# Kernel tuning notes

Measured on AMD Instinct MI355X. Metric: run time of the kernel, lower is better.

The kernel has to match this reference:

```python
import jax, jax.numpy as jnp
import numpy as np

B, DIM, H, W = 64, 256, 5, 5


def setup_inputs() -> dict:
    key = jax.random.key(0)
    k1 = jax.random.fold_in(key, 1)
    feat_map = jax.random.normal(k1, (B, DIM, H, W), dtype=jnp.float32)
    # nn.Parameter init: log(1 / (2 * h * w)) * ones(1, 1)
    temperature = jnp.full((1, 1), float(np.log(1.0 / (2 * H * W))), dtype=jnp.float32)
    return {"feat_map": feat_map, "temperature": temperature}


def reference(feat_map, temperature):
    # comp_relation with lego=False, normalize_bdc=True, out_map=False, no_diag=False
    b, d, h, w = feat_map.shape
    f = feat_map.reshape(b, d, h * w)                     # [B, d, hw]
    # pairwise channel correlation: sum_p |f_i + f_j| - |f_i - f_j|
    s_plus = jnp.sum(jnp.abs(f[:, :, None, :] + f[:, None, :, :]), axis=-1)   # [B, d, d]
    s_minus = jnp.sum(jnp.abs(f[:, :, None, :] - f[:, None, :, :]), axis=-1)  # [B, d, d]
    out = (s_plus - s_minus) * 0.5 * jnp.exp(temperature[0, 0])
    # centering: out - (1/d) out @ ones - (1/d) ones @ out
    row_mean = jnp.sum(out, axis=2, keepdims=True) / d    # (out @ I_M) / d, broadcast over cols
    col_mean = jnp.sum(out, axis=1, keepdims=True) / d    # (I_M @ out) / d, broadcast over rows
    out = out - row_mean - col_mean
    # Triuvec (including diagonal), row-major order as in torch nonzero of triu mask
    iu, ju = jnp.triu_indices(d)
    return out[:, iu, ju]                                 # [B, d*(d+1)/2]
```

## Files before the change

kernel.cpp:

```cpp
#include <hip/hip_runtime.h>
#include <math.h>

#define NB   64
#define D    256
#define HW   25
#define TRI  32896
#define TS   64
#define PSTR 68

__device__ __forceinline__ void tile_bands(int t, int& bi, int& bj) {
    bi = (t < 4) ? 0 : (t < 7) ? 1 : (t < 9) ? 2 : 3;
    const int o4 = (bi == 0) ? 0 : (bi == 1) ? 4 : (bi == 2) ? 7 : 9;
    bj = bi + (t - o4);
}

__global__ __launch_bounds__(256) void tile_kernel(const float* __restrict__ feat,
                                                   float* __restrict__ rsp,
                                                   float* __restrict__ out) {
    __shared__ __align__(16) float as[HW * PSTR];
    __shared__ __align__(16) float bs[HW * PSTR];
    __shared__ float red[2][TS][17];

    const int tid = threadIdx.x;
    const int blk = blockIdx.x;
    const int b   = blk / 10;
    const int t   = blk - b * 10;
    int bi, bj; tile_bands(t, bi, bj);
    const int ibase = bi * TS, jbase = bj * TS;
    const bool diag = (bi == bj);

    const float* fb = feat + (size_t)b * D * HW;

    for (int idx = tid; idx < TS * HW; idx += 256) {
        int r = idx / HW;
        int p = idx - r * HW;
        as[p * PSTR + r] = fb[(ibase + r) * HW + p];
        bs[p * PSTR + r] = fb[(jbase + r) * HW + p];
    }
    __syncthreads();

    const int tx = tid & 15;
    const int ty = tid >> 4;

    float acc[4][4] = {{0.f}};
#pragma unroll 5
    for (int p = 0; p < HW; ++p) {
        float4 av = *reinterpret_cast<const float4*>(&as[p * PSTR + ty * 4]);
        float4 bv = *reinterpret_cast<const float4*>(&bs[p * PSTR + tx * 4]);
        float a4[4] = {av.x, av.y, av.z, av.w};
        float b4[4] = {bv.x, bv.y, bv.z, bv.w};
#pragma unroll
        for (int r = 0; r < 4; ++r)
#pragma unroll
            for (int q = 0; q < 4; ++q)
                acc[r][q] += fabsf(a4[r] + b4[q]) - fabsf(a4[r] - b4[q]);
    }

    float* ob = out + (size_t)b * TRI;
    if (diag) {
#pragma unroll
        for (int r = 0; r < 4; ++r) {
            const int i = ibase + ty * 4 + r;
            const int rowoff = (i * (513 - i)) >> 1;
#pragma unroll
            for (int q = 0; q < 4; ++q) {
                const int j = jbase + tx * 4 + q;
                if (j >= i) ob[rowoff + (j - i)] = acc[r][q];
            }
        }
    } else {
#pragma unroll
        for (int r = 0; r < 4; ++r) {
            const int i = ibase + ty * 4 + r;
            const int rowoff = (i * (513 - i)) >> 1;
#pragma unroll
            for (int q = 0; q < 4; ++q) {
                const int j = jbase + tx * 4 + q;
                ob[rowoff + (j - i)] = acc[r][q];
            }
        }
    }

    float pi[4];
#pragma unroll
    for (int r = 0; r < 4; ++r) pi[r] = acc[r][0] + acc[r][1] + acc[r][2] + acc[r][3];
#pragma unroll
    for (int r = 0; r < 4; ++r) red[0][ty * 4 + r][tx] = pi[r];
    if (!diag) {
        float pj[4];
#pragma unroll
        for (int q = 0; q < 4; ++q) pj[q] = acc[0][q] + acc[1][q] + acc[2][q] + acc[3][q];
#pragma unroll
        for (int q = 0; q < 4; ++q) red[1][tx * 4 + q][ty] = pj[q];
    }
    __syncthreads();

    if (tid < TS) {
        float si = 0.f;
#pragma unroll
        for (int x = 0; x < 16; ++x) si += red[0][tid][x];
        rsp[((b * 4 + bi) * 4 + (bj - bi)) * TS + tid] = si;
        if (!diag) {
            float sj = 0.f;
#pragma unroll
            for (int x = 0; x < 16; ++x) sj += red[1][tid][x];
            rsp[((b * 4 + bj) * 4 + (4 - bj + bi)) * TS + tid] = sj;
        }
    }
}

__global__ __launch_bounds__(256) void center_kernel(const float* __restrict__ temp,
                                                     const float* __restrict__ rsp,
                                                     float* __restrict__ out) {
    __shared__ float rsum[2][TS];

    const int tid = threadIdx.x;
    const int blk = blockIdx.x;
    const int b   = blk / 10;
    const int t   = blk - b * 10;
    int bi, bj; tile_bands(t, bi, bj);
    const int ibase = bi * TS, jbase = bj * TS;
    const bool diag = (bi == bj);

    if (tid < TS) {
        float s = 0.f;
#pragma unroll
        for (int sl = 0; sl < 4; ++sl) s += rsp[((b * 4 + bi) * 4 + sl) * TS + tid];
        rsum[0][tid] = s;
    } else if (tid < 2 * TS) {
        const int il = tid - TS;
        float s = 0.f;
#pragma unroll
        for (int sl = 0; sl < 4; ++sl) s += rsp[((b * 4 + bj) * 4 + sl) * TS + il];
        rsum[1][il] = s;
    }
    __syncthreads();

    const int tx = tid & 15;
    const int ty = tid >> 4;
    const float sc = 0.5f * expf(temp[0]);
    float* ob = out + (size_t)b * TRI;

#pragma unroll
    for (int r = 0; r < 4; ++r) {
        const int i = ibase + ty * 4 + r;
        const int rowoff = (i * (513 - i)) >> 1;
        const float ri = rsum[0][ty * 4 + r];
#pragma unroll
        for (int q = 0; q < 4; ++q) {
            const int j = jbase + tx * 4 + q;
            if (!diag || j >= i) {
                float* p = &ob[rowoff + (j - i)];
                const float e = *p;
                *p = sc * (e - (ri + rsum[1][tx * 4 + q]) * (1.0f / 256.0f));
            }
        }
    }
}

extern "C" void kernel_launch(void* const* d_in, const int* in_sizes, int n_in,
                              void* d_out, int out_size, void* d_ws, size_t ws_size,
                              hipStream_t stream) {
    const float* feat = (const float*)d_in[0];
    const float* temp = (const float*)d_in[1];
    float* out = (float*)d_out;
    float* rsp = (float*)d_ws;

    tile_kernel<<<NB * 10, 256, 0, stream>>>(feat, rsp, out);
    center_kernel<<<NB * 10, 256, 0, stream>>>(temp, rsp, out);
}
```

Measured before the change: 28.54 us.

## Shrink tiles to 32x32 with 64-thread blocks for more parallel blocks

Moves from 64x64 tiles in 256-thread blocks (640 blocks) to 32x32 tiles in 64-thread blocks (2304 blocks), and rewrites the row-sum partial layout and triangular tile mapping to match. Diagonal tiles now reuse the A tile instead of loading B. The aim is to spread the small workload across more CUs and waves and to cut wasted work on diagonal tiles. The cost is more blocks, more redundant global loads of feature rows, and more partial sums to combine in the centering kernel.

Result: slower. 36.49 us (+27.8%).

```diff
diff --git a/kernel.cpp b/kernel.cpp
--- a/kernel.cpp
+++ b/kernel.cpp
@@ -5,48 +5,60 @@
 #define D    256
 #define HW   25
 #define TRI  32896
-#define TS   64
-#define PSTR 68
+#define BTS  32
+#define NT   36
+#define PST  36
 
-__device__ __forceinline__ void tile_bands(int t, int& bi, int& bj) {
-    bi = (t < 4) ? 0 : (t < 7) ? 1 : (t < 9) ? 2 : 3;
-    const int o4 = (bi == 0) ? 0 : (bi == 1) ? 4 : (bi == 2) ? 7 : 9;
-    bj = bi + (t - o4);
+__device__ __forceinline__ void tile_bands8(int t, int& bi, int& bj) {
+    int acc = 0;
+#pragma unroll
+    for (int w = 0; w < 8; ++w) {
+        const int cnt = 8 - w;
+        if (t < acc + cnt) { bi = w; bj = w + (t - acc); return; }
+        acc += cnt;
+    }
+    bi = 7; bj = 7;
 }
 
-__global__ __launch_bounds__(256) void tile_kernel(const float* __restrict__ feat,
-                                                   float* __restrict__ rsp,
-                                                   float* __restrict__ out) {
-    __shared__ __align__(16) float as[HW * PSTR];
-    __shared__ __align__(16) float bs[HW * PSTR];
-    __shared__ float red[2][TS][17];
+__global__ __launch_bounds__(64) void tile_kernel(const float* __restrict__ feat,
+                                                  float* __restrict__ rsp,
+                                                  float* __restrict__ out) {
+    __shared__ __align__(16) float as[HW * PST];
+    __shared__ __align__(16) float bs[HW * PST];
+    __shared__ float red0[BTS][9];
+    __shared__ float red1[BTS][9];
 
     const int tid = threadIdx.x;
     const int blk = blockIdx.x;
-    const int b   = blk / 10;
-    const int t   = blk - b * 10;
-    int bi, bj; tile_bands(t, bi, bj);
-    const int ibase = bi * TS, jbase = bj * TS;
+    const int b   = blk / NT;
+    const int t   = blk - b * NT;
+    int bi, bj; tile_bands8(t, bi, bj);
+    const int ibase = bi * BTS, jbase = bj * BTS;
     const bool diag = (bi == bj);
 
     const float* fb = feat + (size_t)b * D * HW;
 
-    for (int idx = tid; idx < TS * HW; idx += 256) {
-        int r = idx / HW;
-        int p = idx - r * HW;
-        as[p * PSTR + r] = fb[(ibase + r) * HW + p];
-        bs[p * PSTR + r] = fb[(jbase + r) * HW + p];
+    for (int idx = tid; idx < BTS * HW; idx += 64) {
+        const int r = idx / HW, p = idx - r * HW;
+        as[p * PST + r] = fb[(ibase + r) * HW + p];
+    }
+    if (!diag) {
+        for (int idx = tid; idx < BTS * HW; idx += 64) {
+            const int r = idx / HW, p = idx - r * HW;
+            bs[p * PST + r] = fb[(jbase + r) * HW + p];
+        }
     }
     __syncthreads();
 
-    const int tx = tid & 15;
-    const int ty = tid >> 4;
+    const float* bsp = diag ? as : bs;
+    const int tx = tid & 7;
+    const int ty = tid >> 3;
 
     float acc[4][4] = {{0.f}};
-#pragma unroll 5
+#pragma unroll
     for (int p = 0; p < HW; ++p) {
-        float4 av = *reinterpret_cast<const float4*>(&as[p * PSTR + ty * 4]);
-        float4 bv = *reinterpret_cast<const float4*>(&bs[p * PSTR + tx * 4]);
+        float4 av = *reinterpret_cast<const float4*>(&as[p * PST + ty * 4]);
+        float4 bv = *reinterpret_cast<const float4*>(&bsp[p * PST + tx * 4]);
         float a4[4] = {av.x, av.y, av.z, av.w};
         float b4[4] = {bv.x, bv.y, bv.z, bv.w};
 #pragma unroll
@@ -85,59 +97,60 @@
 #pragma unroll
     for (int r = 0; r < 4; ++r) pi[r] = acc[r][0] + acc[r][1] + acc[r][2] + acc[r][3];
 #pragma unroll
-    for (int r = 0; r < 4; ++r) red[0][ty * 4 + r][tx] = pi[r];
+    for (int r = 0; r < 4; ++r) red0[ty * 4 + r][tx] = pi[r];
     if (!diag) {
         float pj[4];
 #pragma unroll
         for (int q = 0; q < 4; ++q) pj[q] = acc[0][q] + acc[1][q] + acc[2][q] + acc[3][q];
 #pragma unroll
-        for (int q = 0; q < 4; ++q) red[1][tx * 4 + q][ty] = pj[q];
+        for (int q = 0; q < 4; ++q) red1[tx * 4 + q][ty] = pj[q];
     }
     __syncthreads();
 
-    if (tid < TS) {
-        float si = 0.f;
+    if (tid < BTS) {
+        float s = 0.f;
 #pragma unroll
-        for (int x = 0; x < 16; ++x) si += red[0][tid][x];
-        rsp[((b * 4 + bi) * 4 + (bj - bi)) * TS + tid] = si;
-        if (!diag) {
-            float sj = 0.f;
+        for (int x = 0; x < 8; ++x) s += red0[tid][x];
+        rsp[((b * 8 + bi) * 8 + (bj - bi)) * BTS + tid] = s;
+    } else if (!diag) {
+        const int c = tid - BTS;
+        float s = 0.f;
 #pragma unroll
-            for (int x = 0; x < 16; ++x) sj += red[1][tid][x];
-            rsp[((b * 4 + bj) * 4 + (4 - bj + bi)) * TS + tid] = sj;
-        }
+        for (int x = 0; x < 8; ++x) s += red1[c][x];
+        rsp[((b * 8 + bj) * 8 + (8 - bj + bi)) * BTS + c] = s;
     }
 }
 
-__global__ __launch_bounds__(256) void center_kernel(const float* __restrict__ temp,
-                                                     const float* __restrict__ rsp,
-                                                     float* __restrict__ out) {
-    __shared__ float rsum[2][TS];
+__global__ __launch_bounds__(64) void center_kernel(const float* __restrict__ temp,
+                                                    const float* __restrict__ rsp,
+                                                    float* __restrict__ out) {
+    __shared__ float rsum0[BTS];
+    __shared__ float rsum1[BTS];
 
     const int tid = threadIdx.x;
     const int blk = blockIdx.x;
-    const int b   = blk / 10;
-    const int t   = blk - b * 10;
-    int bi, bj; tile_bands(t, bi, bj);
-    const int ibase = bi * TS, jbase = bj * TS;
+    const int b   = blk / NT;
+    const int t   = blk - b * NT;
+    int bi, bj; tile_bands8(t, bi, bj);
+    const int ibase = bi * BTS, jbase = bj * BTS;
     const bool diag = (bi == bj);
 
-    if (tid < TS) {
+    if (tid < BTS) {
         float s = 0.f;
 #pragma unroll
-        for (int sl = 0; sl < 4; ++sl) s += rsp[((b * 4 + bi) * 4 + sl) * TS + tid];
-        rsum[0][tid] = s;
-    } else if (tid < 2 * TS) {
-        const int il = tid - TS;
+        for (int sl = 0; sl < 8; ++sl) s += rsp[((b * 8 + bi) * 8 + sl) * BTS + tid];
+        rsum0[tid] = s;
+    } else {
+        const int c = tid - BTS;
         float s = 0.f;
 #pragma unroll
-        for (int sl = 0; sl < 4; ++sl) s += rsp[((b * 4 + bj) * 4 + sl) * TS + il];
-        rsum[1][il] = s;
+        for (int sl = 0; sl < 8; ++sl) s += rsp[((b * 8 + bj) * 8 + sl) * BTS + c];
+        rsum1[c] = s;
     }
     __syncthreads();
 
-    const int tx = tid & 15;
-    const int ty = tid >> 4;
+    const int tx = tid & 7;
+    const int ty = tid >> 3;
     const float sc = 0.5f * expf(temp[0]);
     float* ob = out + (size_t)b * TRI;
 
@@ -145,14 +158,14 @@
     for (int r = 0; r < 4; ++r) {
         const int i = ibase + ty * 4 + r;
         const int rowoff = (i * (513 - i)) >> 1;
-        const float ri = rsum[0][ty * 4 + r];
+        const float ri = rsum0[ty * 4 + r];
 #pragma unroll
         for (int q = 0; q < 4; ++q) {
             const int j = jbase + tx * 4 + q;
             if (!diag || j >= i) {
                 float* p = &ob[rowoff + (j - i)];
                 const float e = *p;
-                *p = sc * (e - (ri + rsum[1][tx * 4 + q]) * (1.0f / 256.0f));
+                *p = sc * (e - (ri + rsum1[tx * 4 + q]) * (1.0f / 256.0f));
             }
         }
     }
@@ -166,6 +179,6 @@
     float* out = (float*)d_out;
     float* rsp = (float*)d_ws;
 
-    tile_kernel<<<NB * 10, 256, 0, stream>>>(feat, rsp, out);
-    center_kernel<<<NB * 10, 256, 0, stream>>>(temp, rsp, out);
+    tile_kernel<<<NB * NT, 64, 0, stream>>>(feat, rsp, out);
+    center_kernel<<<NB * NT, 64, 0, stream>>>(temp, rsp, out);
 }
```

## Fuse tile and centering kernels with per-batch flag barrier across blocks

Applied to the files above, without the earlier changes.

Merges the two kernels into one. The ten tile blocks of each batch exchange readiness through global atomic flags and spin-wait, then apply centering and scaling straight from the register accumulators. This removes the second launch and the write-then-read round trip of the raw correlations through global memory. Diagonal tiles also skip loading a duplicate copy of the B tile. The scheme depends on all ten blocks of a batch being co-resident, which 640 small blocks should satisfy, and on the flags workspace starting at zero.

Result: slower. 55.46 us (+94.3%).

```diff
diff --git a/kernel.cpp b/kernel.cpp
--- a/kernel.cpp
+++ b/kernel.cpp
@@ -7,6 +7,8 @@
 #define TRI  32896
 #define TS   64
 #define PSTR 68
+#define MAGIC 0x13579BDF
+#define SLOT_FLOATS (NB * 4 * 4 * TS)
 
 __device__ __forceinline__ void tile_bands(int t, int& bi, int& bj) {
     bi = (t < 4) ? 0 : (t < 7) ? 1 : (t < 9) ? 2 : 3;
@@ -14,12 +16,15 @@
     bj = bi + (t - o4);
 }
 
-__global__ __launch_bounds__(256) void tile_kernel(const float* __restrict__ feat,
-                                                   float* __restrict__ rsp,
-                                                   float* __restrict__ out) {
+__global__ __launch_bounds__(256) void fused_kernel(const float* __restrict__ feat,
+                                                    const float* __restrict__ temp,
+                                                    float* __restrict__ rsp,
+                                                    int* __restrict__ flags,
+                                                    float* __restrict__ out) {
     __shared__ __align__(16) float as[HW * PSTR];
     __shared__ __align__(16) float bs[HW * PSTR];
     __shared__ float red[2][TS][17];
+    __shared__ float rsum[2][TS];
 
     const int tid = threadIdx.x;
     const int blk = blockIdx.x;
@@ -35,10 +40,17 @@
         int r = idx / HW;
         int p = idx - r * HW;
         as[p * PSTR + r] = fb[(ibase + r) * HW + p];
-        bs[p * PSTR + r] = fb[(jbase + r) * HW + p];
+    }
+    if (!diag) {
+        for (int idx = tid; idx < TS * HW; idx += 256) {
+            int r = idx / HW;
+            int p = idx - r * HW;
+            bs[p * PSTR + r] = fb[(jbase + r) * HW + p];
+        }
     }
     __syncthreads();
 
+    const float* bsp = diag ? as : bs;
     const int tx = tid & 15;
     const int ty = tid >> 4;
 
@@ -46,7 +58,7 @@
 #pragma unroll 5
     for (int p = 0; p < HW; ++p) {
         float4 av = *reinterpret_cast<const float4*>(&as[p * PSTR + ty * 4]);
-        float4 bv = *reinterpret_cast<const float4*>(&bs[p * PSTR + tx * 4]);
+        float4 bv = *reinterpret_cast<const float4*>(&bsp[p * PSTR + tx * 4]);
         float a4[4] = {av.x, av.y, av.z, av.w};
         float b4[4] = {bv.x, bv.y, bv.z, bv.w};
 #pragma unroll
@@ -54,31 +66,6 @@
 #pragma unroll
             for (int q = 0; q < 4; ++q)
                 acc[r][q] += fabsf(a4[r] + b4[q]) - fabsf(a4[r] - b4[q]);
-    }
-
-    float* ob = out + (size_t)b * TRI;
-    if (diag) {
-#pragma unroll
-        for (int r = 0; r < 4; ++r) {
-            const int i = ibase + ty * 4 + r;
-            const int rowoff = (i * (513 - i)) >> 1;
-#pragma unroll
-            for (int q = 0; q < 4; ++q) {
-                const int j = jbase + tx * 4 + q;
-                if (j >= i) ob[rowoff + (j - i)] = acc[r][q];
-            }
-        }
-    } else {
-#pragma unroll
-        for (int r = 0; r < 4; ++r) {
-            const int i = ibase + ty * 4 + r;
-            const int rowoff = (i * (513 - i)) >> 1;
-#pragma unroll
-            for (int q = 0; q < 4; ++q) {
-                const int j = jbase + tx * 4 + q;
-                ob[rowoff + (j - i)] = acc[r][q];
-            }
-        }
     }
 
     float pi[4];
@@ -100,27 +87,28 @@
 #pragma unroll
         for (int x = 0; x < 16; ++x) si += red[0][tid][x];
         rsp[((b * 4 + bi) * 4 + (bj - bi)) * TS + tid] = si;
-        if (!diag) {
-            float sj = 0.f;
+    } else if (tid < 2 * TS && !diag) {
+        const int il = tid - TS;
+        float sj = 0.f;
 #pragma unroll
-            for (int x = 0; x < 16; ++x) sj += red[1][tid][x];
-            rsp[((b * 4 + bj) * 4 + (4 - bj + bi)) * TS + tid] = sj;
-        }
+        for (int x = 0; x < 16; ++x) sj += red[1][il][x];
+        rsp[((b * 4 + bj) * 4 + (4 - bj + bi)) * TS + il] = sj;
     }
-}
 
-__global__ __launch_bounds__(256) void center_kernel(const float* __restrict__ temp,
-                                                     const float* __restrict__ rsp,
-                                                     float* __restrict__ out) {
-    __shared__ float rsum[2][TS];
-
-    const int tid = threadIdx.x;
-    const int blk = blockIdx.x;
-    const int b   = blk / 10;
-    const int t   = blk - b * 10;
-    int bi, bj; tile_bands(t, bi, bj);
-    const int ibase = bi * TS, jbase = bj * TS;
-    const bool diag = (bi == bj);
+    __builtin_amdgcn_fence(__ATOMIC_RELEASE, "agent");
+    __syncthreads();
+    if (tid < 10) {
+        __hip_atomic_store(&flags[(b * 10 + t) * 10 + tid], MAGIC,
+                           __ATOMIC_RELAXED, __HIP_MEMORY_SCOPE_AGENT);
+    }
+    if (tid < 10) {
+        int* w = &flags[(b * 10 + tid) * 10 + t];
+        while (__hip_atomic_load(w, __ATOMIC_RELAXED, __HIP_MEMORY_SCOPE_AGENT) != MAGIC)
+            __builtin_amdgcn_s_sleep(8);
+        __hip_atomic_store(w, 0, __ATOMIC_RELAXED, __HIP_MEMORY_SCOPE_AGENT);
+    }
+    __syncthreads();
+    __builtin_amdgcn_fence(__ATOMIC_ACQUIRE, "agent");
 
     if (tid < TS) {
         float s = 0.f;
@@ -136,23 +124,33 @@
     }
     __syncthreads();
 
-    const int tx = tid & 15;
-    const int ty = tid >> 4;
     const float sc = 0.5f * expf(temp[0]);
     float* ob = out + (size_t)b * TRI;
-
+    if (diag) {
 #pragma unroll
-    for (int r = 0; r < 4; ++r) {
-        const int i = ibase + ty * 4 + r;
-        const int rowoff = (i * (513 - i)) >> 1;
-        const float ri = rsum[0][ty * 4 + r];
+        for (int r = 0; r < 4; ++r) {
+            const int i = ibase + ty * 4 + r;
+            const int rowoff = (i * (513 - i)) >> 1;
+            const float ri = rsum[0][ty * 4 + r];
 #pragma unroll
-        for (int q = 0; q < 4; ++q) {
-            const int j = jbase + tx * 4 + q;
-            if (!diag || j >= i) {
-                float* p = &ob[rowoff + (j - i)];
-                const float e = *p;
-                *p = sc * (e - (ri + rsum[1][tx * 4 + q]) * (1.0f / 256.0f));
+            for (int q = 0; q < 4; ++q) {
+                const int j = jbase + tx * 4 + q;
+                if (j >= i)
+                    ob[rowoff + (j - i)] =
+                        sc * (acc[r][q] - (ri + rsum[1][tx * 4 + q]) * (1.0f / 256.0f));
+            }
+        }
+    } else {
+#pragma unroll
+        for (int r = 0; r < 4; ++r) {
+            const int i = ibase + ty * 4 + r;
+            const int rowoff = (i * (513 - i)) >> 1;
+            const float ri = rsum[0][ty * 4 + r];
+#pragma unroll
+            for (int q = 0; q < 4; ++q) {
+                const int j = jbase + tx * 4 + q;
+                ob[rowoff + (j - i)] =
+                    sc * (acc[r][q] - (ri + rsum[1][tx * 4 + q]) * (1.0f / 256.0f));
             }
         }
     }
@@ -163,9 +161,9 @@
                               hipStream_t stream) {
     const float* feat = (const float*)d_in[0];
     const float* temp = (const float*)d_in[1];
-    float* out = (float*)d_out;
-    float* rsp = (float*)d_ws;
+    float* out   = (float*)d_out;
+    float* rsp   = (float*)d_ws;
+    int*   flags = (int*)((char*)d_ws + SLOT_FLOATS * sizeof(float));
 
-    tile_kernel<<<NB * 10, 256, 0, stream>>>(feat, rsp, out);
-    center_kernel<<<NB * 10, 256, 0, stream>>>(temp, rsp, out);
+    fused_kernel<<<NB * 10, 256, 0, stream>>>(feat, temp, rsp, flags, out);
 }
```
